# Kernel optimization log

Measured on AMD Instinct MI355X. Metric: run time of the kernel, lower is better.

Reference implementation:

```python
import jax, jax.numpy as jnp
import numpy as np

# ---- quantization constants (8-bit, per-tensor affine; representative values) ----
Q_MAX = 255.0
S_IN, Z_IN = 0.05, 128.0      # block input
S1, Z1 = 0.04, 128.0          # after expand 1x1 + hardswish
S2, Z2 = 0.04, 128.0          # after depthwise 5x5 + hardswish
S_SE1, Z_SE1 = 0.03, 128.0    # SE fc1 output
S_SE2, Z_SE2 = 1.0 / 255.0, 0.0  # SE fc2 hardsigmoid output in [0,1]
S_MUL, Z_MUL = 0.04, 128.0    # SE gated activation
S3, Z3 = 0.05, 128.0          # after project 1x1
S_OUT, Z_OUT = 0.06, 128.0    # after residual add
W_SCALE = 0.01                # symmetric per-tensor weight scale (zero_point = 0)
EXP_C = 576                   # expanded channels (depthwise groups)


def conv(x, w, stride=1, padding=0, groups=1):
    return jax.lax.conv_general_dilated(
        x, w, (stride, stride), [(padding, padding), (padding, padding)],
        feature_group_count=groups, dimension_numbers=('NCHW', 'OIHW', 'NCHW'))


def hardswish(x):
    return x * jnp.clip(x + 3.0, 0.0, 6.0) * (1.0 / 6.0)


def hardsigmoid(x):
    return jnp.clip(x + 3.0, 0.0, 6.0) * (1.0 / 6.0)


def qconv(x_q, w_q, b_q, s_in, z_in, s_out, z_out, stride=1, padding=0, groups=1, act=None):
    """Quantized conv: int-domain accumulation (simulated in fp32), fused activation
    on the dequantized accumulator, then requantize to [0, Q_MAX]."""
    acc = conv(x_q - z_in, w_q, stride, padding, groups) + b_q[None, :, None, None]
    deq = acc * (s_in * W_SCALE)  # dequantize accumulator
    if act == 'hardswish':
        deq = hardswish(deq)
    elif act == 'hardsigmoid':
        deq = hardsigmoid(deq)
    return jnp.clip(deq * (1.0 / s_out) + z_out, 0.0, Q_MAX)


def setup_inputs() -> dict:
    key = jax.random.key(0)
    ks = jax.random.split(key, 11)
    def qw(k, shape):  # int8-style symmetric weights stored as fp32 integers
        return jnp.round(jnp.clip(jax.random.normal(k, shape) * 40.0, -127.0, 127.0))
    def qb(k, n):      # int32-style bias in accumulator domain
        return jnp.round(jax.random.normal(k, (n,)) * 500.0)
    return {
        'x':      jnp.round(jax.random.uniform(ks[0], (64, 96, 28, 28)) * Q_MAX),
        'w_exp':  qw(ks[1], (576, 96, 1, 1)),  'b_exp':  qb(ks[2], 576),
        'w_dw':   qw(ks[3], (576, 1, 5, 5)),   'b_dw':   qb(ks[4], 576),
        'w_se1':  qw(ks[5], (144, 576, 1, 1)), 'b_se1':  qb(ks[6], 144),
        'w_se2':  qw(ks[7], (576, 144, 1, 1)), 'b_se2':  qb(ks[8], 576),
        'w_proj': qw(ks[9], (96, 576, 1, 1)),  'b_proj': qb(ks[10], 96),
    }


def reference(x, w_exp, b_exp, w_dw, b_dw, w_se1, b_se1, w_se2, b_se2, w_proj, b_proj):
    # expand 1x1 (+ hardswish)
    e = qconv(x, w_exp, b_exp, S_IN, Z_IN, S1, Z1, act='hardswish')
    # depthwise 5x5, padding=(5-1)//2=2, groups=expanded (+ hardswish)
    d = qconv(e, w_dw, b_dw, S1, Z1, S2, Z2, padding=2, groups=EXP_C, act='hardswish')
    # squeeze-excitation: global avg pool -> fc1 -> fc2(hardsigmoid) -> quantized mul
    pooled = jnp.mean(d, axis=(2, 3), keepdims=True)  # [N, 576, 1, 1]
    g1 = qconv(pooled, w_se1, b_se1, S2, Z2, S_SE1, Z_SE1)
    g2 = qconv(g1, w_se2, b_se2, S_SE1, Z_SE1, S_SE2, Z_SE2, act='hardsigmoid')
    gated = jnp.clip((g2 - Z_SE2) * (d - Z2) * (S_SE2 * S2 / S_MUL) + Z_MUL, 0.0, Q_MAX)
    # project 1x1 (linear)
    p = qconv(gated, w_proj, b_proj, S_MUL, Z_MUL, S3, Z3)
    # quantized residual add (stride=1, in==out channels -> use_res_connect)
    out = jnp.clip((x - Z_IN) * (S_IN / S_OUT) + (p - Z3) * (S3 / S_OUT) + Z_OUT, 0.0, Q_MAX)
    return out
```

## Files before the change

kernel.cpp:

```cpp
#include <hip/hip_runtime.h>

typedef _Float16 v8h __attribute__((ext_vector_type(8)));
typedef _Float16 v4h __attribute__((ext_vector_type(4)));
typedef _Float16 v2h __attribute__((ext_vector_type(2)));
typedef float v4f __attribute__((ext_vector_type(4)));

#define NB 64
#define CI 96
#define CE 576
#define CO 96
#define HW 784
#define SEC 144

#if defined(__has_builtin)
#if __has_builtin(__builtin_amdgcn_fdot2)
#define HAVE_FDOT2 1
#endif
#endif

__device__ __forceinline__ float fdot2(v2h a, v2h b, float c) {
#ifdef HAVE_FDOT2
  return __builtin_amdgcn_fdot2(a, b, c, false);
#else
  return (float)a[0] * (float)b[0] + ((float)a[1] * (float)b[1] + c);
#endif
}

__global__ __launch_bounds__(256) void k0_cvt_w(const float* __restrict__ w_exp,
                                                const float* __restrict__ w_proj,
                                                _Float16* __restrict__ w_exp_h,
                                                _Float16* __restrict__ w_proj_h) {
  int i = blockIdx.x * 256 + threadIdx.x;
  if (i < CE * CI) {
    w_exp_h[i]  = (_Float16)w_exp[i];
    w_proj_h[i] = (_Float16)w_proj[i];
  }
}

__global__ __launch_bounds__(384) void k1_expand(const float* __restrict__ x,
                                                 const _Float16* __restrict__ w_exp_h,
                                                 const float* __restrict__ b_exp,
                                                 _Float16* __restrict__ e_s) {
  __shared__ _Float16 xf[3 * 7 * 520];
  const int tid = threadIdx.x;
  const int n   = blockIdx.z;
  const int co0 = blockIdx.y * 96;
  const int hw0 = blockIdx.x * 112;

#pragma unroll
  for (int it = 0; it < 7; ++it) {
    int idx = it * 384 + tid;
    int c = idx / 28, seg = idx % 28;
    const float4 v = *(const float4*)&x[(n * CI + c) * HW + hw0 + seg * 4];
    int s = c >> 5, q = (c >> 3) & 3, j = c & 7;
    int t = seg >> 2, l0 = (seg & 3) * 4;
    int base = (s * 7 + t) * 520 + (q * 16 + l0) * 8 + j;
    xf[base]      = (_Float16)(v.x - 128.0f);
    xf[base + 8]  = (_Float16)(v.y - 128.0f);
    xf[base + 16] = (_Float16)(v.z - 128.0f);
    xf[base + 24] = (_Float16)(v.w - 128.0f);
  }
  __syncthreads();

  const int wv = tid >> 6, lane = tid & 63;
  const int l15 = lane & 15, q = lane >> 4;

  const _Float16* wrow = &w_exp_h[(co0 + wv * 16 + l15) * CI + q * 8];
  v8h a0 = *(const v8h*)(wrow);
  v8h a1 = *(const v8h*)(wrow + 32);
  v8h a2 = *(const v8h*)(wrow + 64);

  v4f acc[7];
#pragma unroll
  for (int t = 0; t < 7; ++t) acc[t] = (v4f){0.f, 0.f, 0.f, 0.f};

#pragma unroll
  for (int t = 0; t < 7; ++t) {
    v8h b0 = *(const v8h*)&xf[(0 * 7 + t) * 520 + lane * 8];
    v8h b1 = *(const v8h*)&xf[(1 * 7 + t) * 520 + lane * 8];
    v8h b2 = *(const v8h*)&xf[(2 * 7 + t) * 520 + lane * 8];
    acc[t] = __builtin_amdgcn_mfma_f32_16x16x32_f16(a0, b0, acc[t], 0, 0, 0);
    acc[t] = __builtin_amdgcn_mfma_f32_16x16x32_f16(a1, b1, acc[t], 0, 0, 0);
    acc[t] = __builtin_amdgcn_mfma_f32_16x16x32_f16(a2, b2, acc[t], 0, 0, 0);
  }

  float bia[4];
#pragma unroll
  for (int r = 0; r < 4; ++r) bia[r] = b_exp[co0 + wv * 16 + q * 4 + r];

#pragma unroll
  for (int t = 0; t < 7; ++t) {
#pragma unroll
    for (int r = 0; r < 4; ++r) {
      int co = co0 + wv * 16 + q * 4 + r;
      int hw = hw0 + t * 16 + l15;
      float deq = (acc[t][r] + bia[r]) * 5.0e-4f;
      float cl  = fminf(fmaxf(deq + 3.0f, 0.0f), 6.0f);
      float hs  = deq * cl * (1.0f / 6.0f);
      float ev  = fminf(fmaxf(hs * 25.0f, -128.0f), 127.0f);
      e_s[(n * CE + co) * HW + hw] = (_Float16)ev;
    }
  }
}

__global__ __launch_bounds__(256, 4) void k2_dw(const _Float16* __restrict__ e_s,
                                                const float* __restrict__ w_dw,
                                                const float* __restrict__ b_dw,
                                                _Float16* __restrict__ d_t,
                                                float* __restrict__ d_sums) {
  __shared__ _Float16 e_lds[8][32][36];
  __shared__ _Float16 w_pairs[8][5][8];
  __shared__ _Float16 d_tile[784 * 9];
  const int tid = threadIdx.x;
  const int n = blockIdx.y;
  const int c0 = blockIdx.x * 8;

  {
    unsigned long long* z = (unsigned long long*)&e_lds[0][0][0];
    for (int idx = tid; idx < 8 * 32 * 36 * 2 / 8; idx += 256) z[idx] = 0ull;
  }
  for (int idx = tid; idx < 320; idx += 256) {
    int c = idx / 40, r = idx % 40, dy = r / 8, k = r % 8;
    int tap = (k < 4) ? k : (k - 3);
    w_pairs[c][dy][k] = (_Float16)w_dw[(c0 + c) * 25 + dy * 5 + tap];
  }
  __syncthreads();
  for (int idx = tid; idx < 1568; idx += 256) {
    int c = idx / 196, r = idx % 196, y = r / 7, j = r % 7;
    v4h v = *(const v4h*)&e_s[(n * CE + c0 + c) * HW + y * 28 + j * 4];
    *(v4h*)&e_lds[c][2 + y][4 + j * 4] = v;
  }
  __syncthreads();

  const int c = tid >> 5, l = tid & 31;
  v2h W01[5], W23[5], W12[5], W34[5];
  float W0s[5], W4s[5];
#pragma unroll
  for (int dy = 0; dy < 5; ++dy) {
    W01[dy] = *(const v2h*)&w_pairs[c][dy][0];
    W23[dy] = *(const v2h*)&w_pairs[c][dy][2];
    W12[dy] = *(const v2h*)&w_pairs[c][dy][4];
    W34[dy] = *(const v2h*)&w_pairs[c][dy][6];
    W0s[dy] = (float)W01[dy][0];
    W4s[dy] = (float)W34[dy][1];
  }
  const float bc = b_dw[c0 + c];

  float csum = 0.0f;
  if (l < 28) {
    const int y = l;
    v2h P0[5], P1[5], P2[5], P3[5];
#pragma unroll
    for (int dy = 0; dy < 5; ++dy) {
      const _Float16* row = &e_lds[c][y + dy][0];
      P0[dy] = *(const v2h*)(row + 2);
      P1[dy] = *(const v2h*)(row + 4);
      P2[dy] = *(const v2h*)(row + 6);
      P3[dy] = *(const v2h*)(row + 8);
    }
#pragma unroll
    for (int x0 = 0; x0 < 28; x0 += 4) {
      float o0 = bc, o1 = bc, o2 = bc, o3 = bc;
#pragma unroll
      for (int dy = 0; dy < 5; ++dy) {
        o0 = fdot2(P0[dy], W01[dy], o0);
        o0 = fdot2(P1[dy], W23[dy], o0);
        o0 += (float)P2[dy][0] * W4s[dy];
        o1 += (float)P0[dy][1] * W0s[dy];
        o1 = fdot2(P1[dy], W12[dy], o1);
        o1 = fdot2(P2[dy], W34[dy], o1);
        o2 = fdot2(P1[dy], W01[dy], o2);
        o2 = fdot2(P2[dy], W23[dy], o2);
        o2 += (float)P3[dy][0] * W4s[dy];
        o3 += (float)P1[dy][1] * W0s[dy];
        o3 = fdot2(P2[dy], W12[dy], o3);
        o3 = fdot2(P3[dy], W34[dy], o3);
      }
      float oo[4] = {o0, o1, o2, o3};
#pragma unroll
      for (int i = 0; i < 4; ++i) {
        float deq = oo[i] * 4.0e-4f;
        float cl  = fminf(fmaxf(deq + 3.0f, 0.0f), 6.0f);
        float hs  = deq * cl * (1.0f / 6.0f);
        float dvv = fminf(fmaxf(hs * 25.0f, -128.0f), 127.0f);
        d_tile[(y * 28 + x0 + i) * 9 + c] = (_Float16)dvv;
        csum += dvv;
      }
      if (x0 < 24) {
#pragma unroll
        for (int dy = 0; dy < 5; ++dy) {
          const _Float16* row = &e_lds[c][y + dy][0];
          P0[dy] = P2[dy];
          P1[dy] = P3[dy];
          P2[dy] = *(const v2h*)(row + x0 + 10);
          P3[dy] = *(const v2h*)(row + x0 + 12);
        }
      }
    }
  }
#pragma unroll
  for (int m = 16; m >= 1; m >>= 1) csum += __shfl_xor(csum, m);
  if (l == 0) d_sums[n * CE + c0 + c] = csum;

  __syncthreads();
  const size_t obase = ((size_t)n * 72 + (c0 >> 3)) * 784;
  for (int hw = tid; hw < 784; hw += 256) {
    v8h o;
#pragma unroll
    for (int j = 0; j < 8; ++j) o[j] = d_tile[hw * 9 + j];
    *(v8h*)&d_t[(obase + hw) * 8] = o;
  }
}

__global__ __launch_bounds__(256) void k3a_fc1(const float* __restrict__ d_sums,
                                               const float* __restrict__ w_se1,
                                               const float* __restrict__ b_se1,
                                               float* __restrict__ g1) {
  const int tid = threadIdx.x;
  const int wv = tid >> 6, lane = tid & 63;
  const int n = blockIdx.y;
  const int o = blockIdx.x * 4 + wv;
  const float* wrow = &w_se1[o * CE];
  const float* srow = &d_sums[n * CE];
  float p = 0.f;
#pragma unroll
  for (int s = 0; s < 9; ++s) {
    int cc = lane + s * 64;
    p += wrow[cc] * srow[cc];
  }
#pragma unroll
  for (int m = 32; m >= 1; m >>= 1) p += __shfl_xor(p, m);
  if (lane == 0) {
    float deq = (p * (1.0f / 784.0f) + b_se1[o]) * 4.0e-4f;
    g1[n * SEC + o] = fminf(fmaxf(deq * 33.3333333f + 128.0f, 0.0f), 255.0f) - 128.0f;
  }
}

__global__ __launch_bounds__(256) void k3b_fc2(const float* __restrict__ g1,
                                               const float* __restrict__ w_se2,
                                               const float* __restrict__ b_se2,
                                               _Float16* __restrict__ g2h) {
  const int tid = threadIdx.x;
  const int wv = tid >> 6, lane = tid & 63;
  const int n = blockIdx.y;
  const int o = blockIdx.x * 4 + wv;
  const float* wrow = &w_se2[o * SEC];
  const float* grow = &g1[n * SEC];
  float p = wrow[lane] * grow[lane] + wrow[lane + 64] * grow[lane + 64];
  if (lane < 16) p += wrow[lane + 128] * grow[lane + 128];
#pragma unroll
  for (int m = 32; m >= 1; m >>= 1) p += __shfl_xor(p, m);
  if (lane == 0) {
    float deq = (p + b_se2[o]) * 3.0e-4f;
    g2h[n * CE + o] =
        (_Float16)(fminf(fmaxf(deq + 3.0f, 0.0f), 6.0f) * (1.0f / 6.0f));
  }
}

__global__ __launch_bounds__(384) void k4_proj(const _Float16* __restrict__ d_t,
                                               const _Float16* __restrict__ g2h,
                                               const _Float16* __restrict__ w_proj_h,
                                               const float* __restrict__ b_proj,
                                               const float* __restrict__ x,
                                               float* __restrict__ out) {
  const int tid = threadIdx.x;
  const int n = blockIdx.y;
  const int hw0 = blockIdx.x * 112;
  const int wv = tid >> 6, lane = tid & 63;
  const int l15 = lane & 15, q = lane >> 4;

  v4f acc[7];
#pragma unroll
  for (int t = 0; t < 7; ++t) acc[t] = (v4f){0.f, 0.f, 0.f, 0.f};

  const _Float16* dbase = d_t + (((size_t)n * 72 + q) * 784 + hw0 + l15) * 8;
  const _Float16* abase = &w_proj_h[(wv * 16 + l15) * CE + q * 8];
  const _Float16* gbase = &g2h[(size_t)n * CE + q * 8];

  for (int ks = 0; ks < 18; ++ks) {
    v8h a = *(const v8h*)(abase + ks * 32);
    v8h g = *(const v8h*)(gbase + ks * 32);
    v8h ag = a * g;
    const _Float16* dk = dbase + (size_t)ks * (4 * 784 * 8);
#pragma unroll
    for (int t = 0; t < 7; ++t) {
      v8h b = *(const v8h*)(dk + t * (16 * 8));
      acc[t] = __builtin_amdgcn_mfma_f32_16x16x32_f16(ag, b, acc[t], 0, 0, 0);
    }
  }

  float bia[4];
#pragma unroll
  for (int r = 0; r < 4; ++r) bia[r] = b_proj[wv * 16 + q * 4 + r];

#pragma unroll
  for (int t = 0; t < 7; ++t) {
#pragma unroll
    for (int r = 0; r < 4; ++r) {
      int co = wv * 16 + q * 4 + r;
      int hw = hw0 + t * 16 + l15;
      float p = fminf(fmaxf((acc[t][r] + bia[r]) * 4.0e-4f * 20.0f + 128.0f, 0.0f), 255.0f);
      float xv = x[(n * CO + co) * HW + hw];
      float o = (xv - 128.0f) * 0.8333333333f + (p - 128.0f) * 0.8333333333f + 128.0f;
      out[(n * CO + co) * HW + hw] = fminf(fmaxf(o, 0.0f), 255.0f);
    }
  }
}

extern "C" void kernel_launch(void* const* d_in, const int* in_sizes, int n_in,
                              void* d_out, int out_size, void* d_ws, size_t ws_size,
                              hipStream_t stream) {
  const float* x      = (const float*)d_in[0];
  const float* w_exp  = (const float*)d_in[1];
  const float* b_exp  = (const float*)d_in[2];
  const float* w_dw   = (const float*)d_in[3];
  const float* b_dw   = (const float*)d_in[4];
  const float* w_se1  = (const float*)d_in[5];
  const float* b_se1  = (const float*)d_in[6];
  const float* w_se2  = (const float*)d_in[7];
  const float* b_se2  = (const float*)d_in[8];
  const float* w_proj = (const float*)d_in[9];
  const float* b_proj = (const float*)d_in[10];
  float* out = (float*)d_out;

  char* ws = (char*)d_ws;
  const size_t SZ_W  = (size_t)CE * CI * 2;
  const size_t SZ_ED = (size_t)NB * CE * HW * 2;
  const size_t SZ_S  = (size_t)NB * CE * 4;
  _Float16* w_exp_h  = (_Float16*)(ws);
  _Float16* w_proj_h = (_Float16*)(ws + SZ_W);
  _Float16* e_s      = (_Float16*)(ws + 2 * SZ_W);
  _Float16* d_t      = (_Float16*)(ws + 2 * SZ_W + SZ_ED);
  float*    d_sums   = (float*)   (ws + 2 * SZ_W + 2 * SZ_ED);
  float*    g1       = (float*)   (ws + 2 * SZ_W + 2 * SZ_ED + SZ_S);
  _Float16* g2h      = (_Float16*)(ws + 2 * SZ_W + 2 * SZ_ED + 2 * SZ_S);

  k0_cvt_w<<<(CE * CI + 255) / 256, 256, 0, stream>>>(w_exp, w_proj, w_exp_h, w_proj_h);
  k1_expand<<<dim3(7, 6, NB), 384, 0, stream>>>(x, w_exp_h, b_exp, e_s);
  k2_dw<<<dim3(72, NB), 256, 0, stream>>>(e_s, w_dw, b_dw, d_t, d_sums);
  k3a_fc1<<<dim3(36, NB), 256, 0, stream>>>(d_sums, w_se1, b_se1, g1);
  k3b_fc2<<<dim3(144, NB), 256, 0, stream>>>(g1, w_se2, b_se2, g2h);
  k4_proj<<<dim3(7, NB), 384, 0, stream>>>(d_t, g2h, w_proj_h, b_proj, x, out);
}
```

Measured before the change: 197.7 us.

## Restructure depthwise LDS layouts and split projection output channels across blocks

The depthwise kernel now stores its output tile channel-major, so each thread writes a packed 4-wide half vector instead of strided scalar stores. It shifts the padded input rows so window loads become 4-wide LDS reads, and it raises the occupancy hint from 4 to 5. The projection kernel is split into two 48-channel halves per image, using 192-thread blocks on a 3D grid, which doubles the block count. The cost is that the gather of d_tile during the final transpose is now strided, and each projection block reloads the same activation tiles twice.

```diff
diff --git a/kernel.cpp b/kernel.cpp
--- a/kernel.cpp
+++ b/kernel.cpp
@@ -2,6 +2,7 @@
 
 typedef _Float16 v8h __attribute__((ext_vector_type(8)));
 typedef _Float16 v4h __attribute__((ext_vector_type(4)));
+typedef _Float16 v4h_a4 __attribute__((ext_vector_type(4), aligned(4)));
 typedef _Float16 v2h __attribute__((ext_vector_type(2)));
 typedef float v4f __attribute__((ext_vector_type(4)));
 
@@ -103,14 +104,14 @@
   }
 }
 
-__global__ __launch_bounds__(256, 4) void k2_dw(const _Float16* __restrict__ e_s,
+__global__ __launch_bounds__(256, 5) void k2_dw(const _Float16* __restrict__ e_s,
                                                 const float* __restrict__ w_dw,
                                                 const float* __restrict__ b_dw,
                                                 _Float16* __restrict__ d_t,
                                                 float* __restrict__ d_sums) {
   __shared__ _Float16 e_lds[8][32][36];
   __shared__ _Float16 w_pairs[8][5][8];
-  __shared__ _Float16 d_tile[784 * 9];
+  __shared__ _Float16 d_tile[8][784];
   const int tid = threadIdx.x;
   const int n = blockIdx.y;
   const int c0 = blockIdx.x * 8;
@@ -128,7 +129,7 @@
   for (int idx = tid; idx < 1568; idx += 256) {
     int c = idx / 196, r = idx % 196, y = r / 7, j = r % 7;
     v4h v = *(const v4h*)&e_s[(n * CE + c0 + c) * HW + y * 28 + j * 4];
-    *(v4h*)&e_lds[c][2 + y][4 + j * 4] = v;
+    *(v4h_a4*)&e_lds[c][2 + y][6 + j * 4] = v;
   }
   __syncthreads();
 
@@ -153,10 +154,12 @@
 #pragma unroll
     for (int dy = 0; dy < 5; ++dy) {
       const _Float16* row = &e_lds[c][y + dy][0];
-      P0[dy] = *(const v2h*)(row + 2);
-      P1[dy] = *(const v2h*)(row + 4);
-      P2[dy] = *(const v2h*)(row + 6);
-      P3[dy] = *(const v2h*)(row + 8);
+      v4h w01 = *(const v4h*)(row + 4);
+      v4h w23 = *(const v4h*)(row + 8);
+      P0[dy] = (v2h){w01[0], w01[1]};
+      P1[dy] = (v2h){w01[2], w01[3]};
+      P2[dy] = (v2h){w23[0], w23[1]};
+      P3[dy] = (v2h){w23[2], w23[3]};
     }
 #pragma unroll
     for (int x0 = 0; x0 < 28; x0 += 4) {
@@ -176,24 +179,26 @@
         o3 = fdot2(P2[dy], W12[dy], o3);
         o3 = fdot2(P3[dy], W34[dy], o3);
       }
+      v4h dv;
       float oo[4] = {o0, o1, o2, o3};
 #pragma unroll
       for (int i = 0; i < 4; ++i) {
         float deq = oo[i] * 4.0e-4f;
         float cl  = fminf(fmaxf(deq + 3.0f, 0.0f), 6.0f);
-        float hs  = deq * cl * (1.0f / 6.0f);
-        float dvv = fminf(fmaxf(hs * 25.0f, -128.0f), 127.0f);
-        d_tile[(y * 28 + x0 + i) * 9 + c] = (_Float16)dvv;
+        float dvv = fminf(fmaxf(deq * cl * (25.0f / 6.0f), -128.0f), 127.0f);
+        dv[i] = (_Float16)dvv;
         csum += dvv;
       }
+      *(v4h*)&d_tile[c][y * 28 + x0] = dv;
       if (x0 < 24) {
 #pragma unroll
         for (int dy = 0; dy < 5; ++dy) {
           const _Float16* row = &e_lds[c][y + dy][0];
+          v4h nw = *(const v4h*)(row + x0 + 12);
           P0[dy] = P2[dy];
           P1[dy] = P3[dy];
-          P2[dy] = *(const v2h*)(row + x0 + 10);
-          P3[dy] = *(const v2h*)(row + x0 + 12);
+          P2[dy] = (v2h){nw[0], nw[1]};
+          P3[dy] = (v2h){nw[2], nw[3]};
         }
       }
     }
@@ -207,7 +212,7 @@
   for (int hw = tid; hw < 784; hw += 256) {
     v8h o;
 #pragma unroll
-    for (int j = 0; j < 8; ++j) o[j] = d_tile[hw * 9 + j];
+    for (int j = 0; j < 8; ++j) o[j] = d_tile[j][hw];
     *(v8h*)&d_t[(obase + hw) * 8] = o;
   }
 }
@@ -257,14 +262,15 @@
   }
 }
 
-__global__ __launch_bounds__(384) void k4_proj(const _Float16* __restrict__ d_t,
+__global__ __launch_bounds__(192) void k4_proj(const _Float16* __restrict__ d_t,
                                                const _Float16* __restrict__ g2h,
                                                const _Float16* __restrict__ w_proj_h,
                                                const float* __restrict__ b_proj,
                                                const float* __restrict__ x,
                                                float* __restrict__ out) {
   const int tid = threadIdx.x;
-  const int n = blockIdx.y;
+  const int n = blockIdx.z;
+  const int co0 = blockIdx.y * 48;
   const int hw0 = blockIdx.x * 112;
   const int wv = tid >> 6, lane = tid & 63;
   const int l15 = lane & 15, q = lane >> 4;
@@ -274,7 +280,7 @@
   for (int t = 0; t < 7; ++t) acc[t] = (v4f){0.f, 0.f, 0.f, 0.f};
 
   const _Float16* dbase = d_t + (((size_t)n * 72 + q) * 784 + hw0 + l15) * 8;
-  const _Float16* abase = &w_proj_h[(wv * 16 + l15) * CE + q * 8];
+  const _Float16* abase = &w_proj_h[(co0 + wv * 16 + l15) * CE + q * 8];
   const _Float16* gbase = &g2h[(size_t)n * CE + q * 8];
 
   for (int ks = 0; ks < 18; ++ks) {
@@ -291,13 +297,13 @@
 
   float bia[4];
 #pragma unroll
-  for (int r = 0; r < 4; ++r) bia[r] = b_proj[wv * 16 + q * 4 + r];
+  for (int r = 0; r < 4; ++r) bia[r] = b_proj[co0 + wv * 16 + q * 4 + r];
 
 #pragma unroll
   for (int t = 0; t < 7; ++t) {
 #pragma unroll
     for (int r = 0; r < 4; ++r) {
-      int co = wv * 16 + q * 4 + r;
+      int co = co0 + wv * 16 + q * 4 + r;
       int hw = hw0 + t * 16 + l15;
       float p = fminf(fmaxf((acc[t][r] + bia[r]) * 4.0e-4f * 20.0f + 128.0f, 0.0f), 255.0f);
       float xv = x[(n * CO + co) * HW + hw];
@@ -340,5 +346,5 @@
   k2_dw<<<dim3(72, NB), 256, 0, stream>>>(e_s, w_dw, b_dw, d_t, d_sums);
   k3a_fc1<<<dim3(36, NB), 256, 0, stream>>>(d_sums, w_se1, b_se1, g1);
   k3b_fc2<<<dim3(144, NB), 256, 0, stream>>>(g1, w_se2, b_se2, g2h);
-  k4_proj<<<dim3(7, NB), 384, 0, stream>>>(d_t, g2h, w_proj_h, b_proj, x, out);
-}
+  k4_proj<<<dim3(7, 2, NB), 192, 0, stream>>>(d_t, g2h, w_proj_h, b_proj, x, out);
+}
```

Result: faster. 191.7 us (-3.0%).
